# Kernel optimization log

Measured on AMD Instinct MI355X. Metric: run time of the kernel, lower is better.

The kernel has to match this reference:

```python
import jax, jax.numpy as jnp
import numpy as np

NUM_HEADS = 8  # from init_kwargs

def _conv1x1(x, W, b):
    # x: [B, Cin, H, W], W: [Cout, Cin], b: [Cout]  (nn.Conv2d kernel_size=1)
    return jnp.einsum('bchw,oc->bohw', x, W) + b[None, :, None, None]

def setup_inputs() -> dict:
    key = jax.random.key(0)
    ks = jax.random.split(key, 9)
    B, C, H, W = 8, 256, 32, 32
    Ck, Cv, Co = 256, 256, 256
    s = 1.0 / np.sqrt(C)
    return {
        'x':  jax.random.normal(ks[0], (B, C, H, W), dtype=jnp.float32),
        'Wq': jax.random.normal(ks[1], (Ck, C), dtype=jnp.float32) * s,
        'bq': jax.random.normal(ks[2], (Ck,), dtype=jnp.float32) * 0.02,
        'Wk': jax.random.normal(ks[3], (Ck, C), dtype=jnp.float32) * s,
        'bk': jax.random.normal(ks[4], (Ck,), dtype=jnp.float32) * 0.02,
        'Wv': jax.random.normal(ks[5], (Cv, C), dtype=jnp.float32) * s,
        'bv': jax.random.normal(ks[6], (Cv,), dtype=jnp.float32) * 0.02,
        'Wo': jax.random.normal(ks[7], (Co, Cv), dtype=jnp.float32) * s,
        'bo': jax.random.normal(ks[8], (Co,), dtype=jnp.float32) * 0.02,
    }

def reference(x, Wq, bq, Wk, bk, Wv, bv, Wo, bo):
    B, C, H, W = x.shape
    q = _conv1x1(x, Wq, bq)  # [B, Ck, H, W]
    k = _conv1x1(x, Wk, bk)  # [B, Ck, H, W]
    v = _conv1x1(x, Wv, bv)  # [B, Cv, H, W]
    nh = NUM_HEADS
    dk = q.shape[1] // nh
    dv = v.shape[1] // nh
    N = H * W
    # split heads, flatten spatial dims into sequence
    q = q.reshape(B, nh, dk, N) * (dk ** -0.5)
    k = k.reshape(B, nh, dk, N)
    v = v.reshape(B, nh, dv, N)
    logits = jnp.einsum('bhdn,bhdm->bhnm', q, k)        # [B, nh, N, N]
    attn = jax.nn.softmax(logits, axis=-1)
    o = jnp.einsum('bhnm,bhdm->bhdn', attn, v)           # [B, nh, dv, N]
    o = o.reshape(B, nh * dv, H, W)
    return _conv1x1(o, Wo, bo)                           # [B, Co, H, W]
```

## Files before the change

### kernel.cpp

```cpp
#include <hip/hip_runtime.h>
#include <math.h>

typedef unsigned short u16;
typedef __attribute__((ext_vector_type(8))) unsigned short u16x8;
typedef __attribute__((ext_vector_type(8))) short s16x8;
typedef __attribute__((ext_vector_type(4))) float f32x4;

__device__ __forceinline__ float bf2f(u16 u) {
  union { unsigned u; float f; } c; c.u = ((unsigned)u) << 16; return c.f;
}
__device__ __forceinline__ u16 f2bf(float f) {
  union { float f; unsigned u; } c; c.f = f;
  unsigned u = c.u;
  u += 0x7fffu + ((u >> 16) & 1u);
  return (u16)(u >> 16);
}
__device__ __forceinline__ u16x8 ld16(const void* p) { u16x8 v; __builtin_memcpy(&v, p, 16); return v; }
__device__ __forceinline__ void st16(void* p, u16x8 v) { __builtin_memcpy(p, &v, 16); }
__device__ __forceinline__ f32x4 ldf4(const void* p) { f32x4 v; __builtin_memcpy(&v, p, 16); return v; }
__device__ __forceinline__ void stf4(void* p, f32x4 v) { __builtin_memcpy(p, &v, 16); }
__device__ __forceinline__ s16x8 frag16(const void* p) { s16x8 v; __builtin_memcpy(&v, p, 16); return v; }
__device__ __forceinline__ s16x8 pack8(f32x4 lo, f32x4 hi) {
  u16x8 u;
  u[0] = f2bf(lo.x); u[1] = f2bf(lo.y); u[2] = f2bf(lo.z); u[3] = f2bf(lo.w);
  u[4] = f2bf(hi.x); u[5] = f2bf(hi.y); u[6] = f2bf(hi.z); u[7] = f2bf(hi.w);
  s16x8 s; __builtin_memcpy(&s, &u, 16); return s;
}

__global__ __launch_bounds__(256) void r17_qkv(
    const float* __restrict__ x,
    const float* __restrict__ Wq, const float* __restrict__ bq,
    const float* __restrict__ Wk, const float* __restrict__ bk,
    const float* __restrict__ Wv, const float* __restrict__ bv,
    u16* __restrict__ qo, u16* __restrict__ ko, u16* __restrict__ vo)
{
  __shared__ u16 xt[64][264];
  __shared__ u16 wlds[96][40];

  const int t = threadIdx.x;
  const int ntile = blockIdx.x, h = blockIdx.y, b = blockIdx.z;
  const int n0 = ntile * 64;
  const int w = t >> 6, lane = t & 63, l15 = lane & 15, quad = lane >> 4;

  {
    const float* xrow = x + ((size_t)b * 256 + t) * 1024 + n0;
#pragma unroll
    for (int i = 0; i < 64; i += 4) {
      const f32x4 a = ldf4(xrow + i);
      xt[i + 0][t] = f2bf(a.x); xt[i + 1][t] = f2bf(a.y);
      xt[i + 2][t] = f2bf(a.z); xt[i + 3][t] = f2bf(a.w);
    }
  }

  f32x4 acc[6];
#pragma unroll
  for (int i = 0; i < 6; ++i) acc[i] = (f32x4){0.f, 0.f, 0.f, 0.f};

  for (int ks = 0; ks < 8; ++ks) {
    __syncthreads();
    if (t < 192) {
      const int row = t >> 1, half = t & 1;
      const float* M = (row < 32) ? Wq : (row < 64) ? Wk : Wv;
      const float* src = M + (size_t)(h * 32 + (row & 31)) * 256 + ks * 32 + half * 16;
      const f32x4 a = ldf4(src),     b4 = ldf4(src + 4);
      const f32x4 c = ldf4(src + 8), d4 = ldf4(src + 12);
      u16x8 u0, u1;
#pragma unroll
      for (int i = 0; i < 4; ++i) {
        u0[i] = f2bf(a[i]);  u0[4 + i] = f2bf(b4[i]);
        u1[i] = f2bf(c[i]);  u1[4 + i] = f2bf(d4[i]);
      }
      st16(&wlds[row][half * 16], u0);
      st16(&wlds[row][half * 16 + 8], u1);
    }
    __syncthreads();

    const s16x8 bfrag = frag16(&xt[w * 16 + l15][ks * 32 + quad * 8]);
#pragma unroll
    for (int mt = 0; mt < 6; ++mt) {
      const s16x8 af = frag16(&wlds[mt * 16 + l15][quad * 8]);
      acc[mt] = __builtin_amdgcn_mfma_f32_16x16x32_bf16(af, bfrag, acc[mt], 0, 0, 0);
    }
  }

  const size_t bh = (size_t)(b * 8 + h);
  const int n = n0 + w * 16 + l15;
#pragma unroll
  for (int half = 0; half < 2; ++half) {
#pragma unroll
    for (int r = 0; r < 4; ++r) {
      const int d = half * 16 + quad * 4 + r;
      qo[(bh * 1024 + n) * 32 + d] =
          f2bf((acc[half][r] + bq[h * 32 + d]) * 0.17677669529663687f);
      ko[(bh * 1024 + n) * 32 + d] = f2bf(acc[2 + half][r] + bk[h * 32 + d]);
      vo[(bh * 32 + d) * 1024 + n] = f2bf(acc[4 + half][r] + bv[h * 32 + d]);
    }
  }
}

__global__ __launch_bounds__(256) void r17_attn(
    const u16* __restrict__ qw, const u16* __restrict__ kw,
    const u16* __restrict__ vw, float* __restrict__ out)
{
  __shared__ __align__(16) char smem[36352];
  u16 (*klds)[40]  = (u16(*)[40])smem;
  u16 (*vlds)[136] = (u16(*)[136])(smem + 10240);
  u16 (*plds)[136] = (u16(*)[136])(smem + 18944);
  float (*otf)[72] = (float(*)[72])smem;

  const int t = threadIdx.x;
  const int qtile = blockIdx.x;
  const int bh = blockIdx.y;
  const int w = t >> 6, lane = t & 63, l15 = lane & 15, quad = lane >> 4;

  const s16x8 qfrag = frag16(
      qw + ((size_t)bh * 1024 + qtile * 64 + w * 16 + l15) * 32 + quad * 8);

  f32x4 o0 = {0.f, 0.f, 0.f, 0.f}, o1 = {0.f, 0.f, 0.f, 0.f};
  float mrun[4], lrun[4];
#pragma unroll
  for (int r = 0; r < 4; ++r) { mrun[r] = -1e30f; lrun[r] = 0.f; }

  for (int kb = 0; kb < 8; ++kb) {
    {
      const u16* ks_ = kw + ((size_t)bh * 1024 + kb * 128 + (t >> 1)) * 32 + (t & 1) * 16;
      st16(&klds[t >> 1][(t & 1) * 16], ld16(ks_));
      st16(&klds[t >> 1][(t & 1) * 16 + 8], ld16(ks_ + 8));
      const u16* vs_ = vw + ((size_t)bh * 32 + (t >> 3)) * 1024 + kb * 128 + (t & 7) * 16;
      st16(&vlds[t >> 3][(t & 7) * 16], ld16(vs_));
      st16(&vlds[t >> 3][(t & 7) * 16 + 8], ld16(vs_ + 8));
    }
    __syncthreads();

    f32x4 s[8];
    const f32x4 zz = {0.f, 0.f, 0.f, 0.f};
#pragma unroll
    for (int nt2 = 0; nt2 < 8; ++nt2) {
      const s16x8 kf = frag16(&klds[nt2 * 16 + l15][quad * 8]);
      s[nt2] = __builtin_amdgcn_mfma_f32_16x16x32_bf16(qfrag, kf, zz, 0, 0, 0);
    }

#pragma unroll
    for (int r = 0; r < 4; ++r) {
      float mx = s[0][r];
#pragma unroll
      for (int nt2 = 1; nt2 < 8; ++nt2) mx = fmaxf(mx, s[nt2][r]);
      mx = fmaxf(mx, __shfl_xor(mx, 1));
      mx = fmaxf(mx, __shfl_xor(mx, 2));
      mx = fmaxf(mx, __shfl_xor(mx, 4));
      mx = fmaxf(mx, __shfl_xor(mx, 8));
      const float mnew = fmaxf(mrun[r], mx);
      const float alpha = __expf(mrun[r] - mnew);
      float rs = 0.f;
#pragma unroll
      for (int nt2 = 0; nt2 < 8; ++nt2) {
        const float p = __expf(s[nt2][r] - mnew);
        rs += p;
        plds[w * 16 + quad * 4 + r][nt2 * 16 + l15] = f2bf(p);
      }
      rs += __shfl_xor(rs, 1);
      rs += __shfl_xor(rs, 2);
      rs += __shfl_xor(rs, 4);
      rs += __shfl_xor(rs, 8);
      lrun[r] = lrun[r] * alpha + rs;
      mrun[r] = mnew;
      o0[r] *= alpha;
      o1[r] *= alpha;
    }
    __syncthreads();

#pragma unroll
    for (int ks = 0; ks < 4; ++ks) {
      const s16x8 pf  = frag16(&plds[w * 16 + l15][ks * 32 + quad * 8]);
      const s16x8 vf0 = frag16(&vlds[l15][ks * 32 + quad * 8]);
      const s16x8 vf1 = frag16(&vlds[16 + l15][ks * 32 + quad * 8]);
      o0 = __builtin_amdgcn_mfma_f32_16x16x32_bf16(pf, vf0, o0, 0, 0, 0);
      o1 = __builtin_amdgcn_mfma_f32_16x16x32_bf16(pf, vf1, o1, 0, 0, 0);
    }
    __syncthreads();
  }

#pragma unroll
  for (int r = 0; r < 4; ++r) {
    const float inv = 1.0f / lrun[r];
    otf[l15][w * 16 + quad * 4 + r]      = o0[r] * inv;
    otf[16 + l15][w * 16 + quad * 4 + r] = o1[r] * inv;
  }
  __syncthreads();
  {
    const int dd = t >> 3, i = t & 7;
    const int b = bh >> 3, hh = bh & 7;
    float* dst = out + ((size_t)b * 256 + hh * 32 + dd) * 1024 + qtile * 64 + i * 8;
    f32x4 v0, v1;
#pragma unroll
    for (int jj = 0; jj < 4; ++jj) { v0[jj] = otf[dd][i * 8 + jj];
                                     v1[jj] = otf[dd][i * 8 + 4 + jj]; }
    stf4(dst, v0); stf4(dst + 4, v1);
  }
}

__global__ __launch_bounds__(256) void r17_oproj(
    const float* __restrict__ Wo, const float* __restrict__ bo,
    float* __restrict__ out)
{
  __shared__ u16 o2t[32][264];
  const int t = threadIdx.x;
  const int nt = blockIdx.x, b = blockIdx.y;
  const int w = t >> 6, lane = t & 63, l15 = lane & 15, quad = lane >> 4;

  {
    const float* src = out + ((size_t)b * 256 + t) * 1024 + nt * 32;
#pragma unroll
    for (int i = 0; i < 32; i += 4) {
      const f32x4 a = ldf4(src + i);
      o2t[i + 0][t] = f2bf(a.x); o2t[i + 1][t] = f2bf(a.y);
      o2t[i + 2][t] = f2bf(a.z); o2t[i + 3][t] = f2bf(a.w);
    }
  }
  __syncthreads();

  f32x4 acc[4][2];
#pragma unroll
  for (int mt = 0; mt < 4; ++mt) {
    acc[mt][0] = (f32x4){0.f, 0.f, 0.f, 0.f};
    acc[mt][1] = (f32x4){0.f, 0.f, 0.f, 0.f};
  }

  for (int ks = 0; ks < 8; ++ks) {
    const s16x8 b0 = frag16(&o2t[l15][ks * 32 + quad * 8]);
    const s16x8 b1 = frag16(&o2t[16 + l15][ks * 32 + quad * 8]);
#pragma unroll
    for (int mt = 0; mt < 4; ++mt) {
      const float* wsrc = Wo + (size_t)(w * 64 + mt * 16 + l15) * 256 + ks * 32 + quad * 8;
      const s16x8 af = pack8(ldf4(wsrc), ldf4(wsrc + 4));
      acc[mt][0] = __builtin_amdgcn_mfma_f32_16x16x32_bf16(af, b0, acc[mt][0], 0, 0, 0);
      acc[mt][1] = __builtin_amdgcn_mfma_f32_16x16x32_bf16(af, b1, acc[mt][1], 0, 0, 0);
    }
  }

#pragma unroll
  for (int mt = 0; mt < 4; ++mt) {
#pragma unroll
    for (int r = 0; r < 4; ++r) {
      const int oc = w * 64 + mt * 16 + quad * 4 + r;
      const float bov = bo[oc];
      out[((size_t)b * 256 + oc) * 1024 + nt * 32 + l15]      = acc[mt][0][r] + bov;
      out[((size_t)b * 256 + oc) * 1024 + nt * 32 + 16 + l15] = acc[mt][1][r] + bov;
    }
  }
}

extern "C" void kernel_launch(void* const* d_in, const int* in_sizes, int n_in,
                              void* d_out, int out_size, void* d_ws, size_t ws_size,
                              hipStream_t stream) {
  (void)in_sizes; (void)n_in; (void)out_size; (void)ws_size;
  const float* x  = (const float*)d_in[0];
  const float* Wq = (const float*)d_in[1];
  const float* bq = (const float*)d_in[2];
  const float* Wk = (const float*)d_in[3];
  const float* bk = (const float*)d_in[4];
  const float* Wv = (const float*)d_in[5];
  const float* bv = (const float*)d_in[6];
  const float* Wo = (const float*)d_in[7];
  const float* bo = (const float*)d_in[8];
  float* out = (float*)d_out;

  char* ws = (char*)d_ws;
  u16* qw = (u16*)(ws);
  u16* kw = (u16*)(ws + (4u << 20));
  u16* vw = (u16*)(ws + (8u << 20));

  r17_qkv<<<dim3(16, 8, 8), 256, 0, stream>>>(
      x, Wq, bq, Wk, bk, Wv, bv, qw, kw, vw);
  r17_attn<<<dim3(16, 64), 256, 0, stream>>>(qw, kw, vw, out);
  r17_oproj<<<dim3(32, 8), 256, 0, stream>>>(Wo, bo, out);
}
```

Before: 152.0 us.

## Use packed bf16 converts, exp2 softmax, two heads per QKV block, permuted V layout

```diff
diff --git a/kernel.cpp b/kernel.cpp
--- a/kernel.cpp
+++ b/kernel.cpp
@@ -6,28 +6,29 @@
 typedef __attribute__((ext_vector_type(8))) short s16x8;
 typedef __attribute__((ext_vector_type(4))) float f32x4;
 
-__device__ __forceinline__ float bf2f(u16 u) {
-  union { unsigned u; float f; } c; c.u = ((unsigned)u) << 16; return c.f;
-}
-__device__ __forceinline__ u16 f2bf(float f) {
-  union { float f; unsigned u; } c; c.f = f;
-  unsigned u = c.u;
-  u += 0x7fffu + ((u >> 16) & 1u);
-  return (u16)(u >> 16);
-}
+#define QK_SCALE (0.17677669529663687f * 1.4426950408889634f)
+
+__device__ __forceinline__ unsigned cvt2(float lo, float hi) {
+  unsigned r;
+  asm("v_cvt_pk_bf16_f32 %0, %1, %2" : "=v"(r) : "v"(lo), "v"(hi));
+  return r;
+}
+__device__ __forceinline__ u16 f2bf(float f) { return (u16)cvt2(f, f); }
 __device__ __forceinline__ u16x8 ld16(const void* p) { u16x8 v; __builtin_memcpy(&v, p, 16); return v; }
 __device__ __forceinline__ void st16(void* p, u16x8 v) { __builtin_memcpy(p, &v, 16); }
+__device__ __forceinline__ void st16s(void* p, s16x8 v) { __builtin_memcpy(p, &v, 16); }
+__device__ __forceinline__ void st4(void* p, unsigned v) { __builtin_memcpy(p, &v, 4); }
 __device__ __forceinline__ f32x4 ldf4(const void* p) { f32x4 v; __builtin_memcpy(&v, p, 16); return v; }
 __device__ __forceinline__ void stf4(void* p, f32x4 v) { __builtin_memcpy(p, &v, 16); }
 __device__ __forceinline__ s16x8 frag16(const void* p) { s16x8 v; __builtin_memcpy(&v, p, 16); return v; }
 __device__ __forceinline__ s16x8 pack8(f32x4 lo, f32x4 hi) {
-  u16x8 u;
-  u[0] = f2bf(lo.x); u[1] = f2bf(lo.y); u[2] = f2bf(lo.z); u[3] = f2bf(lo.w);
-  u[4] = f2bf(hi.x); u[5] = f2bf(hi.y); u[6] = f2bf(hi.z); u[7] = f2bf(hi.w);
-  s16x8 s; __builtin_memcpy(&s, &u, 16); return s;
-}
-
-__global__ __launch_bounds__(256) void r17_qkv(
+  union { unsigned u[4]; s16x8 s; } c;
+  c.u[0] = cvt2(lo.x, lo.y); c.u[1] = cvt2(lo.z, lo.w);
+  c.u[2] = cvt2(hi.x, hi.y); c.u[3] = cvt2(hi.z, hi.w);
+  return c.s;
+}
+
+__global__ __launch_bounds__(256) void r18_qkv(
     const float* __restrict__ x,
     const float* __restrict__ Wq, const float* __restrict__ bq,
     const float* __restrict__ Wk, const float* __restrict__ bk,
@@ -35,11 +36,11 @@
     u16* __restrict__ qo, u16* __restrict__ ko, u16* __restrict__ vo)
 {
   __shared__ u16 xt[64][264];
-  __shared__ u16 wlds[96][40];
+  __shared__ u16 wlds[192][40];
 
   const int t = threadIdx.x;
-  const int ntile = blockIdx.x, h = blockIdx.y, b = blockIdx.z;
-  const int n0 = ntile * 64;
+  const int ntile = blockIdx.x, hp = blockIdx.y, b = blockIdx.z;
+  const int n0 = ntile * 64, h0 = hp * 2;
   const int w = t >> 6, lane = t & 63, l15 = lane & 15, quad = lane >> 4;
 
   {
@@ -52,53 +53,64 @@
     }
   }
 
-  f32x4 acc[6];
-#pragma unroll
-  for (int i = 0; i < 6; ++i) acc[i] = (f32x4){0.f, 0.f, 0.f, 0.f};
+  f32x4 acc[12];
+#pragma unroll
+  for (int i = 0; i < 12; ++i) acc[i] = (f32x4){0.f, 0.f, 0.f, 0.f};
 
   for (int ks = 0; ks < 8; ++ks) {
     __syncthreads();
     if (t < 192) {
-      const int row = t >> 1, half = t & 1;
-      const float* M = (row < 32) ? Wq : (row < 64) ? Wk : Wv;
-      const float* src = M + (size_t)(h * 32 + (row & 31)) * 256 + ks * 32 + half * 16;
-      const f32x4 a = ldf4(src),     b4 = ldf4(src + 4);
-      const f32x4 c = ldf4(src + 8), d4 = ldf4(src + 12);
-      u16x8 u0, u1;
-#pragma unroll
-      for (int i = 0; i < 4; ++i) {
-        u0[i] = f2bf(a[i]);  u0[4 + i] = f2bf(b4[i]);
-        u1[i] = f2bf(c[i]);  u1[4 + i] = f2bf(d4[i]);
-      }
-      st16(&wlds[row][half * 16], u0);
-      st16(&wlds[row][half * 16 + 8], u1);
+      const int m = t >> 6, hh = (t >> 5) & 1, r = t & 31;
+      const float* M = (m == 0) ? Wq : (m == 1) ? Wk : Wv;
+      const float* src = M + (size_t)((h0 + hh) * 32 + r) * 256 + ks * 32;
+      st16s(&wlds[t][0],  pack8(ldf4(src),      ldf4(src + 4)));
+      st16s(&wlds[t][8],  pack8(ldf4(src + 8),  ldf4(src + 12)));
+      st16s(&wlds[t][16], pack8(ldf4(src + 16), ldf4(src + 20)));
+      st16s(&wlds[t][24], pack8(ldf4(src + 24), ldf4(src + 28)));
     }
     __syncthreads();
 
     const s16x8 bfrag = frag16(&xt[w * 16 + l15][ks * 32 + quad * 8]);
 #pragma unroll
-    for (int mt = 0; mt < 6; ++mt) {
+    for (int mt = 0; mt < 12; ++mt) {
       const s16x8 af = frag16(&wlds[mt * 16 + l15][quad * 8]);
       acc[mt] = __builtin_amdgcn_mfma_f32_16x16x32_bf16(af, bfrag, acc[mt], 0, 0, 0);
     }
   }
 
-  const size_t bh = (size_t)(b * 8 + h);
   const int n = n0 + w * 16 + l15;
-#pragma unroll
-  for (int half = 0; half < 2; ++half) {
-#pragma unroll
-    for (int r = 0; r < 4; ++r) {
-      const int d = half * 16 + quad * 4 + r;
-      qo[(bh * 1024 + n) * 32 + d] =
-          f2bf((acc[half][r] + bq[h * 32 + d]) * 0.17677669529663687f);
-      ko[(bh * 1024 + n) * 32 + d] = f2bf(acc[2 + half][r] + bk[h * 32 + d]);
-      vo[(bh * 32 + d) * 1024 + n] = f2bf(acc[4 + half][r] + bv[h * 32 + d]);
-    }
-  }
-}
-
-__global__ __launch_bounds__(256) void r17_attn(
+  const int sig = n & 127;
+  const int nperm = (n & ~127) | ((sig & 15) << 3) | (sig >> 4);
+#pragma unroll
+  for (int hh = 0; hh < 2; ++hh) {
+    const int h = h0 + hh;
+    const size_t bh = (size_t)(b * 8 + h);
+    u16* qrow = qo + (bh * 1024 + n) * 32;
+    u16* krow = ko + (bh * 1024 + n) * 32;
+#pragma unroll
+    for (int half = 0; half < 2; ++half) {
+      const int d0 = half * 16 + quad * 4;
+      const f32x4 aq = acc[hh * 2 + half];
+      const f32x4 ak = acc[4 + hh * 2 + half];
+      const f32x4 av = acc[8 + hh * 2 + half];
+      st4(qrow + d0,     cvt2((aq.x + bq[h * 32 + d0 + 0]) * QK_SCALE,
+                              (aq.y + bq[h * 32 + d0 + 1]) * QK_SCALE));
+      st4(qrow + d0 + 2, cvt2((aq.z + bq[h * 32 + d0 + 2]) * QK_SCALE,
+                              (aq.w + bq[h * 32 + d0 + 3]) * QK_SCALE));
+      st4(krow + d0,     cvt2(ak.x + bk[h * 32 + d0 + 0],
+                              ak.y + bk[h * 32 + d0 + 1]));
+      st4(krow + d0 + 2, cvt2(ak.z + bk[h * 32 + d0 + 2],
+                              ak.w + bk[h * 32 + d0 + 3]));
+#pragma unroll
+      for (int rr = 0; rr < 4; ++rr) {
+        const int d = d0 + rr;
+        vo[(bh * 32 + d) * 1024 + nperm] = f2bf(av[rr] + bv[h * 32 + d]);
+      }
+    }
+  }
+}
+
+__global__ __launch_bounds__(256) void r18_attn(
     const u16* __restrict__ qw, const u16* __restrict__ kw,
     const u16* __restrict__ vw, float* __restrict__ out)
 {
@@ -142,22 +154,22 @@
 
 #pragma unroll
     for (int r = 0; r < 4; ++r) {
-      float mx = s[0][r];
-#pragma unroll
-      for (int nt2 = 1; nt2 < 8; ++nt2) mx = fmaxf(mx, s[nt2][r]);
+      float mx = fmaxf(fmaxf(fmaxf(s[0][r], s[1][r]), fmaxf(s[2][r], s[3][r])),
+                       fmaxf(fmaxf(s[4][r], s[5][r]), fmaxf(s[6][r], s[7][r])));
       mx = fmaxf(mx, __shfl_xor(mx, 1));
       mx = fmaxf(mx, __shfl_xor(mx, 2));
       mx = fmaxf(mx, __shfl_xor(mx, 4));
       mx = fmaxf(mx, __shfl_xor(mx, 8));
       const float mnew = fmaxf(mrun[r], mx);
-      const float alpha = __expf(mrun[r] - mnew);
-      float rs = 0.f;
-#pragma unroll
-      for (int nt2 = 0; nt2 < 8; ++nt2) {
-        const float p = __expf(s[nt2][r] - mnew);
-        rs += p;
-        plds[w * 16 + quad * 4 + r][nt2 * 16 + l15] = f2bf(p);
+      const float alpha = exp2f(mrun[r] - mnew);
+      f32x4 plo, phi;
+#pragma unroll
+      for (int j = 0; j < 4; ++j) {
+        plo[j] = exp2f(s[j][r] - mnew);
+        phi[j] = exp2f(s[4 + j][r] - mnew);
       }
+      float rs = ((plo.x + plo.y) + (plo.z + plo.w)) +
+                 ((phi.x + phi.y) + (phi.z + phi.w));
       rs += __shfl_xor(rs, 1);
       rs += __shfl_xor(rs, 2);
       rs += __shfl_xor(rs, 4);
@@ -166,8 +178,8 @@
       mrun[r] = mnew;
       o0[r] *= alpha;
       o1[r] *= alpha;
-    }
-    __syncthreads();
+      st16s(&plds[w * 16 + quad * 4 + r][l15 * 8], pack8(plo, phi));
+    }
 
 #pragma unroll
     for (int ks = 0; ks < 4; ++ks) {
@@ -199,7 +211,7 @@
   }
 }
 
-__global__ __launch_bounds__(256) void r17_oproj(
+__global__ __launch_bounds__(256) void r18_oproj(
     const float* __restrict__ Wo, const float* __restrict__ bo,
     float* __restrict__ out)
 {
@@ -270,8 +282,8 @@
   u16* kw = (u16*)(ws + (4u << 20));
   u16* vw = (u16*)(ws + (8u << 20));
 
-  r17_qkv<<<dim3(16, 8, 8), 256, 0, stream>>>(
+  r18_qkv<<<dim3(16, 4, 8), 256, 0, stream>>>(
       x, Wq, bq, Wk, bk, Wv, bv, qw, kw, vw);
-  r17_attn<<<dim3(16, 64), 256, 0, stream>>>(qw, kw, vw, out);
-  r17_oproj<<<dim3(32, 8), 256, 0, stream>>>(Wo, bo, out);
-}
+  r18_attn<<<dim3(16, 64), 256, 0, stream>>>(qw, kw, vw, out);
+  r18_oproj<<<dim3(32, 8), 256, 0, stream>>>(Wo, bo, out);
+}
```

Measured after the change: 151.0 us. No clear change (-0.7%).
